# Kernel tuning notes

Hardware: AMD Instinct MI355X
Metric: run time of the kernel (lower is better)

The kernel has to match this reference:

```python
import jax, jax.numpy as jnp
import numpy as np

B, E, H, K, C, N = 4096, 768, 2048, 128, 200, 20


def _ln(x, g, b, eps=1e-5):
    m = x.mean(-1, keepdims=True)
    v = jnp.mean((x - m) ** 2, axis=-1, keepdims=True)
    return (x - m) / jnp.sqrt(v + eps) * g + b


def _sn(W):
    # spectral_norm parametrization at eval: divide by top singular value
    return W / jnp.linalg.norm(W, ord=2)


def setup_inputs() -> dict:
    key = jax.random.key(0)
    ks = jax.random.split(key, 8)
    return {
        "features": jax.random.normal(ks[0], (B, E), dtype=jnp.float32),
        "ln1_g": jnp.ones((E,), jnp.float32),
        "ln1_b": jnp.zeros((E,), jnp.float32),
        "W1": jax.random.normal(ks[1], (H, E), jnp.float32) * 0.02,
        "b1": jnp.zeros((H,), jnp.float32),
        "ln2_g": jnp.ones((H,), jnp.float32),
        "ln2_b": jnp.zeros((H,), jnp.float32),
        "W2": jax.random.normal(ks[2], (H, H), jnp.float32) * 0.02,
        "b2": jnp.zeros((H,), jnp.float32),
        "Wp": jax.random.normal(ks[3], (K, H), jnp.float32) * 0.02,
        "bp": jnp.zeros((K,), jnp.float32),
        "log_lengthscale": jnp.zeros((), jnp.float32),  # log(1.0)
        "inducing_points": jax.random.normal(ks[4], (C, N, K), jnp.float32) * 0.1,
        "variational_mean": jax.random.normal(ks[5], (C, N), jnp.float32) * 0.01,
    }


def reference(features, ln1_g, ln1_b, W1, b1, ln2_g, ln2_b, W2, b2, Wp, bp,
              log_lengthscale, inducing_points, variational_mean):
    # SN-MLP feature extractor (dropout=0 at eval)
    h = _ln(features, ln1_g, ln1_b)
    h = jax.nn.gelu(h @ _sn(W1).T + b1, approximate=False)
    h = _ln(h, ln2_g, ln2_b)
    h = jax.nn.gelu(h @ _sn(W2).T + b2, approximate=False)
    h = h @ _sn(Wp).T + bp  # [B, K]

    n_ind = inducing_points.shape[1]
    ls2 = jnp.exp(2.0 * log_lengthscale)
    z = inducing_points  # [C, N, K]

    # RBF kernels via squared distances (batched over classes)
    h2 = jnp.sum(h * h, axis=-1)            # [B]
    z2 = jnp.sum(z * z, axis=-1)            # [C, N]
    hz = jnp.einsum('bk,cnk->cbn', h, z)    # [C, B, N]
    d2_xz = jnp.maximum(h2[None, :, None] + z2[:, None, :] - 2.0 * hz, 0.0)
    k_xz = jnp.exp(-d2_xz / (2.0 * ls2))    # [C, B, N]

    zz = jnp.einsum('cnk,cmk->cnm', z, z)   # [C, N, N]
    d2_zz = jnp.maximum(z2[:, :, None] + z2[:, None, :] - 2.0 * zz, 0.0)
    k_zz = jnp.exp(-d2_zz / (2.0 * ls2)) + 1e-4 * jnp.eye(n_ind, dtype=h.dtype)

    L = jnp.linalg.cholesky(k_zz)           # [C, N, N]
    cho = jax.vmap(lambda Lc, mc: jax.scipy.linalg.cho_solve((Lc, True), mc))
    alpha = cho(L, variational_mean)        # [C, N]
    logits = jnp.einsum('cbn,cn->bc', k_xz, alpha)  # [B, C]

    tri = jax.vmap(lambda Lc, kc: jax.scipy.linalg.solve_triangular(Lc, kc.T, lower=True))
    v = tri(L, k_xz)                        # [C, N, B]
    var_c = jnp.maximum(1.0 - jnp.sum(v * v, axis=1), 0.0)  # [C, B]
    uncertainty = var_c.mean(axis=0)        # [B]

    probs = jax.nn.softmax(logits, axis=-1)
    return probs, logits, uncertainty
```

## Files before the change

kernel.cpp:

```cpp
#include <hip/hip_runtime.h>
#include <cstdint>
#include <cstddef>

#define NB 4096
#define NE 768
#define NH 2048
#define NKF 128
#define NC 200
#define NN 20
#define NITER_R 8

typedef __attribute__((ext_vector_type(8))) short s16x8;
typedef __attribute__((ext_vector_type(8))) unsigned short u16x8;
typedef __attribute__((ext_vector_type(4))) unsigned short u16x4;
typedef __attribute__((ext_vector_type(4))) float f32x4;

__device__ inline unsigned short f2bf(float x) {
  unsigned u = __builtin_bit_cast(unsigned, x);
  u += 0x7fffu + ((u >> 16) & 1u);
  return (unsigned short)(u >> 16);
}
__device__ inline float bf2f(unsigned short h) {
  return __builtin_bit_cast(float, (unsigned)h << 16);
}
__device__ inline float gelu_exact(float x) {
  return x * 0.5f * (1.0f + erff(x * 0.70710678118654752f));
}

__device__ inline void gl16(const unsigned short* g, unsigned short* l) {
  __builtin_amdgcn_global_load_lds(
      (const __attribute__((address_space(1))) unsigned int*)(uintptr_t)(g),
      (__attribute__((address_space(3))) unsigned int*)(uintptr_t)(l),
      16, 0, 0);
}

constexpr size_t SZ_W1BF = (size_t)NH * NE * 2;
constexpr size_t SZ_W2BF = (size_t)NH * NH * 2;
constexpr size_t SZ_WPBF = (size_t)NKF * NH * 2;
constexpr size_t SZ_SLOT = (size_t)NB * NH * 2;

constexpr size_t OFF_W1BF = 0;
constexpr size_t OFF_W2BF = OFF_W1BF + SZ_W1BF;
constexpr size_t OFF_WPBF = OFF_W2BF + SZ_W2BF;
constexpr size_t OFF_XBF  = OFF_WPBF + SZ_WPBF;
constexpr size_t OFF_H2BF = OFF_XBF;
constexpr size_t OFF_H1BF = OFF_XBF + SZ_SLOT;
constexpr size_t OFF_H1N  = OFF_H1BF + SZ_SLOT;
constexpr size_t OFF_HP   = OFF_H1N + SZ_SLOT;
constexpr size_t OFF_H2S  = OFF_HP + (size_t)NB * NKF * 4;
constexpr size_t OFF_PV   = OFF_H2S + (size_t)NB * 4;
constexpr size_t OFF_SINV = OFF_PV + (size_t)3 * 3 * 2048 * 4;
constexpr size_t OFF_Z2   = OFF_SINV + 256;
constexpr size_t OFF_LC   = OFF_Z2 + (size_t)NC * NN * 4;
constexpr size_t OFF_AL   = OFF_LC + (size_t)NC * NN * NN * 4;
constexpr size_t WS_NEED  = OFF_AL + (size_t)NC * NN * 4;

constexpr size_t GOFF_W1T   = OFF_XBF;
constexpr size_t GOFF_Q0    = GOFF_W1T + (size_t)NE * NH * 2;
constexpr size_t GOFF_Q1    = GOFF_Q0 + (size_t)NE * NE * 2;
constexpr size_t GOFF_GPACC = GOFF_Q1 + (size_t)NE * NE * 2;
constexpr size_t GOFF_G1SA  = GOFF_GPACC + (size_t)NKF * NKF * 4;
constexpr size_t GOFF_G1SB  = GOFF_G1SA + (size_t)NE * NE * 2;
constexpr size_t OFF_XBF2   = GOFF_G1SB + (size_t)NE * NE * 2;
static_assert(OFF_XBF2 + (size_t)NB * NE * 2 <= OFF_XBF + SZ_SLOT, "slotA overflow");
constexpr size_t GOFF_G2SA = OFF_H1BF;
constexpr size_t GOFF_G2SB = OFF_H1BF + (size_t)NH * NH * 2;
constexpr size_t GOFF_P0 = OFF_H1N;
constexpr size_t GOFF_P1 = OFF_H1N + (size_t)NH * NH * 2;
constexpr size_t OFF_HPBF = OFF_H1BF;
constexpr size_t OFF_ZPAD = OFF_H1BF + (size_t)NB * NKF * 2;
constexpr size_t OFF_LGT  = OFF_H1N;
constexpr size_t OFF_VART = OFF_LGT + (size_t)NC * NB * 4;
static_assert(OFF_VART + (size_t)NC * NB * 4 <= OFF_H1N + SZ_SLOT, "slotC overflow");

__global__ __launch_bounds__(256) void prep_all(const float* __restrict__ X,
                                                const float* __restrict__ g1,
                                                const float* __restrict__ be1,
                                                const float* __restrict__ W1,
                                                const float* __restrict__ W2,
                                                const float* __restrict__ Wp,
                                                unsigned short* __restrict__ W1T,
                                                unsigned short* __restrict__ W1bf,
                                                unsigned short* __restrict__ W2bf,
                                                unsigned short* __restrict__ Wpbf,
                                                unsigned short* __restrict__ Xbf,
                                                float* __restrict__ Hp,
                                                float* __restrict__ Gpacc,
                                                float* __restrict__ slots) {
  int b = blockIdx.x, t = threadIdx.x;
  if (b < 384) {
    __shared__ float tile[64][65];
    int bx = b % 12, by = b / 12;
    int c0 = bx * 64, r0 = by * 64;
    int tx = t & 63, ty = t >> 6;
    #pragma unroll
    for (int j = 0; j < 16; ++j) {
      int r = ty + j * 4;
      float v = W1[(size_t)(r0 + r) * NE + c0 + tx];
      tile[r][tx] = v;
      W1bf[(size_t)(r0 + r) * NE + c0 + tx] = f2bf(v);
    }
    __syncthreads();
    #pragma unroll
    for (int j = 0; j < 16; ++j) {
      int cc = ty + j * 4;
      W1T[(size_t)(c0 + cc) * NH + r0 + tx] = f2bf(tile[tx][cc]);
    }
  } else if (b < 896) {
    const int n2v = (NH * NH) / 4;
    const int npv = (NKF * NH) / 4;
    int idx = (b - 384) * 256 + t;
    const int stride = 512 * 256;
    for (int i = idx; i < n2v + npv; i += stride) {
      const float* src; unsigned short* dst; int off;
      if (i < n2v) { src = W2; dst = W2bf; off = i; }
      else         { src = Wp; dst = Wpbf; off = i - n2v; }
      float4 v = *(const float4*)(src + (size_t)off * 4);
      u16x4 o;
      o[0] = f2bf(v.x); o[1] = f2bf(v.y); o[2] = f2bf(v.z); o[3] = f2bf(v.w);
      *(u16x4*)(dst + (size_t)off * 4) = o;
    }
  } else if (b < 1920) {
    int wid = t >> 6, lane = t & 63;
    int row = (b - 896) * 4 + wid;
    const float* xr = X + (size_t)row * NE;
    float4 v[3];
    float s = 0.f, sq = 0.f;
    #pragma unroll
    for (int j = 0; j < 3; ++j) {
      v[j] = *(const float4*)(xr + j * 256 + lane * 4);
      s += v[j].x + v[j].y + v[j].z + v[j].w;
      sq += v[j].x * v[j].x + v[j].y * v[j].y + v[j].z * v[j].z + v[j].w * v[j].w;
    }
    for (int off = 32; off; off >>= 1) { s += __shfl_down(s, off); sq += __shfl_down(sq, off); }
    s = __shfl(s, 0); sq = __shfl(sq, 0);
    float mean = s * (1.0f / NE);
    float var = sq * (1.0f / NE) - mean * mean;
    float rstd = rsqrtf(var + 1e-5f);
    unsigned short* orow = Xbf + (size_t)row * NE;
    #pragma unroll
    for (int j = 0; j < 3; ++j) {
      int e0 = j * 256 + lane * 4;
      float4 gg = *(const float4*)(g1 + e0);
      float4 bb = *(const float4*)(be1 + e0);
      u16x4 o;
      o[0] = f2bf((v[j].x - mean) * rstd * gg.x + bb.x);
      o[1] = f2bf((v[j].y - mean) * rstd * gg.y + bb.y);
      o[2] = f2bf((v[j].z - mean) * rstd * gg.z + bb.z);
      o[3] = f2bf((v[j].w - mean) * rstd * gg.w + bb.w);
      *(u16x4*)(orow + e0) = o;
    }
  } else if (b < 1984) {
    float4 z = {0.f, 0.f, 0.f, 0.f};
    int base = (b - 1920) * 2048 + t;
    #pragma unroll
    for (int q = 0; q < 8; ++q) *((float4*)Hp + base + q * 256) = z;
  } else if (b < 1988) {
    float4 z = {0.f, 0.f, 0.f, 0.f};
    int base = (b - 1984) * 1024 + t;
    #pragma unroll
    for (int q = 0; q < 4; ++q) *((float4*)Gpacc + base + q * 256) = z;
  } else {
    if (t < 32) slots[t] = 0.f;
  }
}

__global__ __launch_bounds__(256) void gemm_multi(const unsigned short* __restrict__ A1, int K1,
                                                  unsigned short* __restrict__ O1a,
                                                  unsigned short* __restrict__ O1b,
                                                  const unsigned short* __restrict__ A2, int K2,
                                                  unsigned short* __restrict__ O2a,
                                                  unsigned short* __restrict__ O2b,
                                                  float cscale) {
  __shared__ __align__(16) unsigned short As[2][128 * 32];
  __shared__ __align__(16) unsigned short Bs[2][128 * 32];
  __shared__ __align__(16) unsigned short Tb[64][136];
  int b = blockIdx.x, t = threadIdx.x;
  const unsigned short* A;
  unsigned short* Cout;
  int Kk, Nn, kb, ke, ti;
  if (b < 42) {
    int kz = b / 21; ti = b % 21;
    A = A1; Kk = K1; Nn = NE;
    Cout = kz ? O1b : O1a;
    kb = kz * (K1 / 2); ke = kb + K1 / 2;
  } else {
    int idx = b - 42;
    int kz = idx / 136; ti = idx % 136;
    A = A2; Kk = K2; Nn = NH;
    Cout = kz ? O2b : O2a;
    kb = kz * (K2 / 2); ke = kb + K2 / 2;
  }
  int ri = 0;
  while ((ri + 1) * (ri + 2) / 2 <= ti) ++ri;
  int rj = ti - ri * (ri + 1) / 2;
  int bm0 = ri * 128, bn0 = rj * 128;

  int wid = t >> 6, lane = t & 63;
  int wm = wid >> 1, wn = wid & 1;
  f32x4 acc[4][4] = {};

  int lrow = t >> 2;
  int lk8 = (((t & 3) ^ ((t >> 3) & 3)) * 8);
  const unsigned short* Ag = A + (size_t)(bm0 + lrow) * Kk + lk8;
  const unsigned short* Bg = A + (size_t)(bn0 + lrow) * Kk + lk8;

  int arow = wm * 64 + (lane & 15);
  int brow = wn * 64 + (lane & 15);
  int kca = (((lane >> 4) ^ ((arow >> 1) & 3)) * 8);
  int kcb = (((lane >> 4) ^ ((brow >> 1) & 3)) * 8);

  #define STAGEM(nb, koff)                                  \
    do {                                                    \
      gl16(Ag + (koff), &As[nb][wid * 512]);                \
      gl16(Ag + (size_t)64 * Kk + (koff), &As[nb][2048 + wid * 512]); \
      gl16(Bg + (koff), &Bs[nb][wid * 512]);                \
      gl16(Bg + (size_t)64 * Kk + (koff), &Bs[nb][2048 + wid * 512]); \
    } while (0)

  STAGEM(0, kb);
  __syncthreads();
  int cb = 0;
  for (int ks = kb; ks < ke; ks += 32) {
    if (ks + 32 < ke) STAGEM(cb ^ 1, ks + 32);
    s16x8 af[4], bfr[4];
    #pragma unroll
    for (int i = 0; i < 4; ++i) af[i] = *(const s16x8*)&As[cb][(arow + i * 16) * 32 + kca];
    #pragma unroll
    for (int j = 0; j < 4; ++j) bfr[j] = *(const s16x8*)&Bs[cb][(brow + j * 16) * 32 + kcb];
    #pragma unroll
    for (int i = 0; i < 4; ++i)
      #pragma unroll
      for (int j = 0; j < 4; ++j)
        acc[i][j] = __builtin_amdgcn_mfma_f32_16x16x32_bf16(af[i], bfr[j], acc[i][j], 0, 0, 0);
    __syncthreads();
    cb ^= 1;
  }
  #undef STAGEM

  int crow0 = bm0 + wm * 64 + (lane >> 4) * 4;
  int ccol0 = bn0 + wn * 64 + (lane & 15);
  #pragma unroll
  for (int i = 0; i < 4; ++i)
    #pragma unroll
    for (int j = 0; j < 4; ++j) {
      int col = ccol0 + j * 16;
      #pragma unroll
      for (int r = 0; r < 4; ++r) {
        int row = crow0 + i * 16 + r;
        Cout[(size_t)row * Nn + col] = f2bf(acc[i][j][r] * cscale);
      }
    }

  if (bm0 != bn0) {
    #pragma unroll
    for (int h = 0; h < 2; ++h) {
      __syncthreads();
      if (wn == h) {
        #pragma unroll
        for (int i = 0; i < 4; ++i)
          #pragma unroll
          for (int j = 0; j < 4; ++j) {
            int lc = j * 16 + (lane & 15);
            #pragma unroll
            for (int r = 0; r < 4; ++r) {
              int lr = wm * 64 + i * 16 + (lane >> 4) * 4 + r;
              Tb[lc][lr] = f2bf(acc[i][j][r] * cscale);
            }
          }
      }
      __syncthreads();
      int c = t >> 2;
      int rs = (t & 3) * 32;
      unsigned short* dst = Cout + (size_t)(bn0 + h * 64 + c) * Nn + bm0 + rs;
      #pragma unroll
      for (int q = 0; q < 4; ++q) *(u16x8*)(dst + q * 8) = *(const u16x8*)&Tb[c][rs + q * 8];
    }
  }
}

__global__ __launch_bounds__(256) void add2(const unsigned short* __restrict__ Q0,
                                            const unsigned short* __restrict__ Q1,
                                            unsigned short* __restrict__ G1o,
                                            const unsigned short* __restrict__ P0,
                                            const unsigned short* __restrict__ P1,
                                            unsigned short* __restrict__ G2o) {
  const int n1 = (NE * NE) / 8;
  const int n2 = (NH * NH) / 8;
  int idx = blockIdx.x * 256 + threadIdx.x;
  for (int i = idx; i < n1 + n2; i += gridDim.x * 256) {
    const unsigned short *a, *bb; unsigned short* o; int off;
    if (i < n1) { a = Q0; bb = Q1; o = G1o; off = i; }
    else        { a = P0; bb = P1; o = G2o; off = i - n1; }
    u16x8 x = *(const u16x8*)(a + (size_t)off * 8);
    u16x8 y = *(const u16x8*)(bb + (size_t)off * 8);
    u16x8 r;
    #pragma unroll
    for (int q = 0; q < 8; ++q) r[q] = f2bf(bf2f(x[q]) + bf2f(y[q]));
    *(u16x8*)(o + (size_t)off * 8) = r;
  }
}

__global__ __launch_bounds__(256) void gram_iter(const unsigned short* __restrict__ Q0,
                                                 const unsigned short* __restrict__ Q1,
                                                 const unsigned short* __restrict__ P0,
                                                 const unsigned short* __restrict__ P1,
                                                 float* __restrict__ vb,
                                                 float* __restrict__ slots, int iter) {
  int b = blockIdx.x, t = threadIdx.x;
  int m, r0, Kd;
  const unsigned short *ga, *gb;
  if (b < 96) { m = 0; ga = Q0; gb = Q1; Kd = NE; r0 = b * 8; }
  else        { m = 1; ga = P0; gb = P1; Kd = NH; r0 = (b - 96) * 8; }

  const float* vin = vb + ((size_t)m * 2 + (iter & 1)) * 2048;
  float* vout      = vb + ((size_t)m * 2 + ((iter + 1) & 1)) * 2048;

  __shared__ float vs[2048];
  for (int k = t; k < Kd; k += 256) vs[k] = (iter == 0) ? 1.0f : vin[k];
  __syncthreads();

  int w = t >> 6, lane = t & 63;
  float nrm = 0.f;
  #pragma unroll
  for (int rr = 0; rr < 2; ++rr) {
    int row = r0 + w * 2 + rr;
    const unsigned short* g0 = ga + (size_t)row * Kd;
    const unsigned short* g1 = gb + (size_t)row * Kd;
    float s = 0.f;
    for (int k0 = lane * 8; k0 < Kd; k0 += 512) {
      u16x8 u = *(const u16x8*)(g0 + k0);
      u16x8 u2 = *(const u16x8*)(g1 + k0);
      #pragma unroll
      for (int q = 0; q < 8; ++q) s += (bf2f(u[q]) + bf2f(u2[q])) * vs[k0 + q];
    }
    for (int off = 32; off; off >>= 1) s += __shfl_down(s, off);
    if (lane == 0) { vout[row] = s; nrm += s * s; }
  }
  if (lane == 0) atomicAdd(&slots[m * 16 + iter + 1], nrm);
}

__global__ __launch_bounds__(256) void gp_power(const float* __restrict__ Gp,
                                                float* __restrict__ sinv) {
  __shared__ float v[NKF];
  __shared__ float pred[8][NKF];
  __shared__ float nacc[2];
  int t = threadIdx.x;
  int rg = (t & 31) * 4;
  int ks = t >> 5;
  f32x4 Greg[16];
  #pragma unroll
  for (int kk = 0; kk < 16; ++kk)
    Greg[kk] = *(const f32x4*)(Gp + (size_t)(ks * 16 + kk) * NKF + rg);
  if (t < NKF) v[t] = 1.0f;
  __syncthreads();
  float s_last0 = 1.f, s_last1 = 1.f;
  for (int it = 0; it < 40; ++it) {
    f32x4 p = {0.f, 0.f, 0.f, 0.f};
    #pragma unroll
    for (int kq = 0; kq < 4; ++kq) {
      f32x4 vv = *(const f32x4*)&v[ks * 16 + kq * 4];
      p += Greg[kq * 4 + 0] * vv[0];
      p += Greg[kq * 4 + 1] * vv[1];
      p += Greg[kq * 4 + 2] * vv[2];
      p += Greg[kq * 4 + 3] * vv[3];
    }
    *(f32x4*)&pred[ks][rg] = p;
    __syncthreads();
    float s = 0.f;
    if (t < NKF) {
      #pragma unroll
      for (int q = 0; q < 8; ++q) s += pred[q][t];
      v[t] = s;
    }
    if (it >= 38) {
      float q2 = (t < NKF) ? s * s : 0.f;
      #pragma unroll
      for (int off = 32; off; off >>= 1) q2 += __shfl_down(q2, off);
      if (t == 0) nacc[0] = q2;
      if (t == 64) nacc[1] = q2;
    }
    __syncthreads();
    if (it == 38 && t == 0) s_last0 = nacc[0] + nacc[1];
    if (it == 39 && t == 0) s_last1 = nacc[0] + nacc[1];
  }
  if (t == 0) sinv[2] = powf(s_last1 / s_last0, -0.25f);
}

__global__ __launch_bounds__(256) void ln_h(const unsigned short* __restrict__ X,
                                            const float* __restrict__ g,
                                            const float* __restrict__ b,
                                            unsigned short* __restrict__ out) {
  int wid = threadIdx.x >> 6, lane = threadIdx.x & 63;
  int row = blockIdx.x * 4 + wid;
  const unsigned short* xr = X + (size_t)row * NH;
  float xv[32];
  float s = 0.f, sq = 0.f;
  #pragma unroll
  for (int j = 0; j < 4; ++j) {
    u16x8 u = *(const u16x8*)(xr + j * 512 + lane * 8);
    #pragma unroll
    for (int q = 0; q < 8; ++q) {
      float x = bf2f(u[q]);
      xv[j * 8 + q] = x; s += x; sq += x * x;
    }
  }
  for (int off = 32; off; off >>= 1) { s += __shfl_down(s, off); sq += __shfl_down(sq, off); }
  s = __shfl(s, 0); sq = __shfl(sq, 0);
  float mean = s * (1.0f / NH);
  float var = sq * (1.0f / NH) - mean * mean;
  float rstd = rsqrtf(var + 1e-5f);
  unsigned short* orow = out + (size_t)row * NH;
  #pragma unroll
  for (int j = 0; j < 4; ++j) {
    int e0 = j * 512 + lane * 8;
    float4 ga = *(const float4*)(g + e0);
    float4 gb = *(const float4*)(g + e0 + 4);
    float4 ba = *(const float4*)(b + e0);
    float4 bb = *(const float4*)(b + e0 + 4);
    u16x8 o;
    o[0] = f2bf((xv[j*8+0] - mean) * rstd * ga.x + ba.x);
    o[1] = f2bf((xv[j*8+1] - mean) * rstd * ga.y + ba.y);
    o[2] = f2bf((xv[j*8+2] - mean) * rstd * ga.z + ba.z);
    o[3] = f2bf((xv[j*8+3] - mean) * rstd * ga.w + ba.w);
    o[4] = f2bf((xv[j*8+4] - mean) * rstd * gb.x + bb.x);
    o[5] = f2bf((xv[j*8+5] - mean) * rstd * gb.y + bb.y);
    o[6] = f2bf((xv[j*8+6] - mean) * rstd * gb.z + bb.z);
    o[7] = f2bf((xv[j*8+7] - mean) * rstd * gb.w + bb.w);
    *(u16x8*)(orow + e0) = o;
  }
}

template <int EPI>
__global__ __launch_bounds__(256) void gemm_nt(const unsigned short* __restrict__ A,
                                               const unsigned short* __restrict__ Bm,
                                               const float* __restrict__ bias,
                                               void* __restrict__ Cout,
                                               int M, int Nn, int Kk, int KCH,
                                               const float* __restrict__ sig, int sigmode) {
  __shared__ __align__(16) unsigned short As[2][128 * 32];
  __shared__ __align__(16) unsigned short Bs[2][128 * 32];
  int t = threadIdx.x;
  int bm0 = blockIdx.x * 128, bn0 = blockIdx.y * 128;
  int wid = t >> 6, lane = t & 63;
  int wm = wid >> 1, wn = wid & 1;

  int kb = 0, ke = Kk;
  if (KCH > 0) { kb = blockIdx.z * KCH; ke = kb + KCH; }

  f32x4 acc[4][4] = {};

  int lrow = t >> 2;
  int lk8 = (((t & 3) ^ ((t >> 3) & 3)) * 8);
  const unsigned short* Ag = A + (size_t)(bm0 + lrow) * Kk + lk8;
  const unsigned short* Bg = Bm + (size_t)(bn0 + lrow) * Kk + lk8;

  int arow = wm * 64 + (lane & 15);
  int brow = wn * 64 + (lane & 15);
  int kca = (((lane >> 4) ^ ((arow >> 1) & 3)) * 8);
  int kcb = (((lane >> 4) ^ ((brow >> 1) & 3)) * 8);

  #define STAGE(nb, koff)                                   \
    do {                                                    \
      gl16(Ag + (koff), &As[nb][wid * 512]);                \
      gl16(Ag + (size_t)64 * Kk + (koff), &As[nb][2048 + wid * 512]); \
      gl16(Bg + (koff), &Bs[nb][wid * 512]);                \
      gl16(Bg + (size_t)64 * Kk + (koff), &Bs[nb][2048 + wid * 512]); \
    } while (0)

  STAGE(0, kb);
  __syncthreads();
  int cb = 0;
  for (int ks = kb; ks < ke; ks += 32) {
    if (ks + 32 < ke) STAGE(cb ^ 1, ks + 32);
    s16x8 af[4], bfr[4];
    #pragma unroll
    for (int i = 0; i < 4; ++i) af[i] = *(const s16x8*)&As[cb][(arow + i * 16) * 32 + kca];
    #pragma unroll
    for (int j = 0; j < 4; ++j) bfr[j] = *(const s16x8*)&Bs[cb][(brow + j * 16) * 32 + kcb];
    #pragma unroll
    for (int i = 0; i < 4; ++i)
      #pragma unroll
      for (int j = 0; j < 4; ++j)
        acc[i][j] = __builtin_amdgcn_mfma_f32_16x16x32_bf16(af[i], bfr[j], acc[i][j], 0, 0, 0);
    __syncthreads();
    cb ^= 1;
  }
  #undef STAGE

  float sc = 1.0f;
  if (sigmode == 1) sc = powf(16.0f * sqrtf(sig[NITER_R] / sig[NITER_R - 1]), -0.125f);
  else if (sigmode == 2) sc = sig[0];

  int crow0 = bm0 + wm * 64 + (lane >> 4) * 4;
  int ccol0 = bn0 + wn * 64 + (lane & 15);
  if constexpr (EPI == 0) {
    unsigned short* C = (unsigned short*)Cout;
    #pragma unroll
    for (int i = 0; i < 4; ++i) {
      #pragma unroll
      for (int j = 0; j < 4; ++j) {
        int col = ccol0 + j * 16;
        float bb = bias[col];
        #pragma unroll
        for (int r = 0; r < 4; ++r) {
          int row = crow0 + i * 16 + r;
          float x = acc[i][j][r] * sc + bb;
          C[(size_t)row * Nn + col] = f2bf(gelu_exact(x));
        }
      }
    }
  } else {
    float* C = (float*)Cout;
    #pragma unroll
    for (int i = 0; i < 4; ++i)
      #pragma unroll
      for (int j = 0; j < 4; ++j) {
        int col = ccol0 + j * 16;
        #pragma unroll
        for (int r = 0; r < 4; ++r) {
          int row = crow0 + i * 16 + r;
          atomicAdd(&C[(size_t)row * Nn + col], acc[i][j][r] * sc);
        }
      }
  }
}

__global__ __launch_bounds__(256) void finish_proj(const float* __restrict__ Hp,
                                                   const float* __restrict__ bp,
                                                   unsigned short* __restrict__ Hpb,
                                                   float* __restrict__ h2) {
  int wid = threadIdx.x >> 6, lane = threadIdx.x & 63;
  int row = blockIdx.x * 4 + wid;
  const float* r = Hp + (size_t)row * NKF;
  float x0 = r[lane] + bp[lane];
  float x1 = r[lane + 64] + bp[lane + 64];
  float s = x0 * x0 + x1 * x1;
  for (int off = 32; off; off >>= 1) s += __shfl_down(s, off);
  unsigned short* hb = Hpb + (size_t)row * NKF;
  hb[lane] = f2bf(x0);
  hb[lane + 64] = f2bf(x1);
  if (lane == 0) h2[row] = s;
}

__global__ __launch_bounds__(128) void gp_prep(const float* __restrict__ z,
                                               const float* __restrict__ vm,
                                               const float* __restrict__ ll,
                                               float* __restrict__ z2g,
                                               float* __restrict__ Lig,
                                               float* __restrict__ alphag,
                                               unsigned short* __restrict__ zpad) {
  int c = blockIdx.x, t = threadIdx.x;
  __shared__ float zc[NN * NKF];
  __shared__ float Amat[NN][NN + 1];
  __shared__ float Li[NN][NN + 1];
  __shared__ float z2s[NN], ys[NN], al[NN];
  const float* zcg = z + (size_t)c * NN * NKF;
  for (int i = t; i < NN * NKF; i += 128) zc[i] = zcg[i];
  __syncthreads();
  if (t < NN) {
    float s = 0.f;
    for (int k = 0; k < NKF; ++k) { float v = zc[t * NKF + k]; s += v * v; }
    z2s[t] = s;
    z2g[c * NN + t] = s;
  }
  __syncthreads();
  float inv2 = 0.5f * expf(-2.0f * ll[0]);
  for (int e = t; e < NN * NN; e += 128) {
    int n = e / NN, m = e % NN;
    float d = 0.f;
    for (int k = 0; k < NKF; ++k) d += zc[n * NKF + k] * zc[m * NKF + k];
    float d2 = fmaxf(z2s[n] + z2s[m] - 2.0f * d, 0.0f);
    float v = expf(-d2 * inv2);
    if (n == m) v += 1e-4f;
    Amat[n][m] = v;
  }
  __syncthreads();
  for (int j = 0; j < NN; ++j) {
    if (t == 0) {
      float s = Amat[j][j];
      for (int p = 0; p < j; ++p) s -= Amat[j][p] * Amat[j][p];
      Amat[j][j] = sqrtf(s);
    }
    __syncthreads();
    if (t > j && t < NN) {
      float s = Amat[t][j];
      for (int p = 0; p < j; ++p) s -= Amat[t][p] * Amat[j][p];
      Amat[t][j] = s / Amat[j][j];
    }
    __syncthreads();
  }
  if (t < NN) {
    int j = t;
    for (int n = 0; n < NN; ++n) {
      float s;
      if (n < j) s = 0.f;
      else {
        s = (n == j) ? 1.f : 0.f;
        for (int m = j; m < n; ++m) s -= Amat[n][m] * Li[m][j];
        s /= Amat[n][n];
      }
      Li[n][j] = s;
    }
  }
  if (t == 0) {
    const float* mc = vm + c * NN;
    for (int n = 0; n < NN; ++n) {
      float s = mc[n];
      for (int m = 0; m < n; ++m) s -= Amat[n][m] * ys[m];
      ys[n] = s / Amat[n][n];
    }
    for (int n = NN - 1; n >= 0; --n) {
      float s = ys[n];
      for (int m = n + 1; m < NN; ++m) s -= Amat[m][n] * al[m];
      al[n] = s / Amat[n][n];
    }
  }
  __syncthreads();
  for (int e = t; e < NN * NN; e += 128)
    Lig[(size_t)c * NN * NN + e] = Li[e / NN][e % NN];
  if (t < NN) alphag[c * NN + t] = al[t];
  unsigned short* zp = zpad + (size_t)c * 32 * NKF;
  for (int i = t; i < 32 * NKF; i += 128) {
    int n = i >> 7;
    zp[i] = (n < NN) ? f2bf(zc[n * NKF + (i & 127)]) : (unsigned short)0;
  }
}

__global__ __launch_bounds__(256) void gp_main(const unsigned short* __restrict__ Hpb,
                                               const float* __restrict__ h2g,
                                               const unsigned short* __restrict__ zpad,
                                               const float* __restrict__ z2g,
                                               const float* __restrict__ Lig,
                                               const float* __restrict__ alphag,
                                               const float* __restrict__ ll,
                                               float* __restrict__ logitsT,
                                               float* __restrict__ varT) {
  int c = blockIdx.y, b0 = blockIdx.x * 256, t = threadIdx.x;
  int w = t >> 6, lane = t & 63;
  __shared__ __align__(16) unsigned short zs[32 * 136];
  __shared__ float kxs[256][21];
  __shared__ float Ls[NN][21];
  __shared__ float z2s[32], al[NN], ht2[256];

  {
    const unsigned short* zp = zpad + (size_t)c * 32 * NKF;
    int n = t >> 3, k = (t & 7) * 16;
    u16x8 a = *(const u16x8*)(zp + n * NKF + k);
    u16x8 b = *(const u16x8*)(zp + n * NKF + k + 8);
    *(u16x8*)&zs[n * 136 + k] = a;
    *(u16x8*)&zs[n * 136 + k + 8] = b;
  }
  for (int i = t; i < NN * NN; i += 256) Ls[i / NN][i % NN] = Lig[(size_t)c * NN * NN + i];
  if (t < 32) z2s[t] = (t < NN) ? z2g[c * NN + t] : 0.f;
  if (t < NN) al[t] = alphag[c * NN + t];
  ht2[t] = h2g[b0 + t];
  float inv2 = 0.5f * __expf(-2.0f * ll[0]);
  __syncthreads();

  f32x4 acc[4][2] = {};
  const unsigned short* hbase = Hpb + (size_t)(b0 + w * 64 + (lane & 15)) * NKF + (lane >> 4) * 8;
  #pragma unroll
  for (int ks = 0; ks < 4; ++ks) {
    s16x8 af[4], bfr[2];
    #pragma unroll
    for (int i = 0; i < 4; ++i) af[i] = *(const s16x8*)(hbase + (size_t)i * 16 * NKF + ks * 32);
    #pragma unroll
    for (int j = 0; j < 2; ++j)
      bfr[j] = *(const s16x8*)&zs[(j * 16 + (lane & 15)) * 136 + ks * 32 + (lane >> 4) * 8];
    #pragma unroll
    for (int i = 0; i < 4; ++i)
      #pragma unroll
      for (int j = 0; j < 2; ++j)
        acc[i][j] = __builtin_amdgcn_mfma_f32_16x16x32_bf16(af[i], bfr[j], acc[i][j], 0, 0, 0);
  }

  #pragma unroll
  for (int i = 0; i < 4; ++i)
    #pragma unroll
    for (int j = 0; j < 2; ++j) {
      int col = j * 16 + (lane & 15);
      #pragma unroll
      for (int r = 0; r < 4; ++r) {
        int rl = w * 64 + i * 16 + (lane >> 4) * 4 + r;
        float d2 = fmaxf(ht2[rl] + z2s[col] - 2.0f * acc[i][j][r], 0.0f);
        float kx = __expf(-d2 * inv2);
        if (col < NN) kxs[rl][col] = kx;
      }
    }
  __syncthreads();

  float kr[NN];
  #pragma unroll
  for (int n = 0; n < NN; ++n) kr[n] = kxs[t][n];
  float lg = 0.f;
  #pragma unroll
  for (int n = 0; n < NN; ++n) lg += kr[n] * al[n];
  logitsT[(size_t)c * NB + b0 + t] = lg;

  float vsum = 0.f;
  #pragma unroll
  for (int n = 0; n < NN; ++n) {
    float wv = 0.f;
    #pragma unroll
// ... 23 lines not shown
    vs += varT[(size_t)cc * NB + b0 + j];
  }
  redmx[p][j] = mx;
  redvs[p][j] = vs;
  __syncthreads();
  if (p == 0) {
    mxs[j] = fmaxf(fmaxf(redmx[0][j], redmx[1][j]), fmaxf(redmx[2][j], redmx[3][j]));
    unc[b0 + j] = (redvs[0][j] + redvs[1][j] + redvs[2][j] + redvs[3][j]) * (1.0f / NC);
  }
  __syncthreads();
  float m2 = mxs[j], sm = 0.f;
  for (int cc = p * 50; cc < p * 50 + 50; ++cc) sm += __expf(tile[cc][j] - m2);
  redsm[p][j] = sm;
  __syncthreads();
  if (p == 0) invs[j] = 1.0f / (redsm[0][j] + redsm[1][j] + redsm[2][j] + redsm[3][j]);
  __syncthreads();
  for (int i = t; i < 64 * NC; i += 256) {
    int jj = i / NC, cc = i % NC;
    float lv = tile[cc][jj];
    size_t o = (size_t)(b0 + jj) * NC + cc;
    probs[o] = __expf(lv - mxs[jj]) * invs[jj];
    logits_out[o] = lv;
  }
}

extern "C" void kernel_launch(void* const* d_in, const int* in_sizes, int n_in,
                              void* d_out, int out_size, void* d_ws, size_t ws_size,
                              hipStream_t stream) {
  if (ws_size < WS_NEED) return;

  const float* X   = (const float*)d_in[0];
  const float* g1  = (const float*)d_in[1];
  const float* be1 = (const float*)d_in[2];
  const float* W1  = (const float*)d_in[3];
  const float* b1  = (const float*)d_in[4];
  const float* g2  = (const float*)d_in[5];
  const float* be2 = (const float*)d_in[6];
  const float* W2  = (const float*)d_in[7];
  const float* b2  = (const float*)d_in[8];
  const float* Wp  = (const float*)d_in[9];
  const float* bp  = (const float*)d_in[10];
  const float* ll  = (const float*)d_in[11];
  const float* Z   = (const float*)d_in[12];
  const float* VM  = (const float*)d_in[13];

  char* ws = (char*)d_ws;
  unsigned short* W1bf = (unsigned short*)(ws + OFF_W1BF);
  unsigned short* W2bf = (unsigned short*)(ws + OFF_W2BF);
  unsigned short* Wpbf = (unsigned short*)(ws + OFF_WPBF);
  unsigned short* Xbf  = (unsigned short*)(ws + OFF_XBF2);
  unsigned short* H2bf = (unsigned short*)(ws + OFF_H2BF);
  unsigned short* H1bf = (unsigned short*)(ws + OFF_H1BF);
  unsigned short* H1n  = (unsigned short*)(ws + OFF_H1N);
  float* Hp    = (float*)(ws + OFF_HP);
  float* h2s   = (float*)(ws + OFF_H2S);
  float* vb    = (float*)(ws + OFF_PV);
  float* slots = vb + 2 * 2 * 2048;
  float* sinv  = (float*)(ws + OFF_SINV);
  float* z2g   = (float*)(ws + OFF_Z2);
  float* Lg    = (float*)(ws + OFF_LC);
  float* alphag= (float*)(ws + OFF_AL);

  unsigned short* W1T  = (unsigned short*)(ws + GOFF_W1T);
  unsigned short* Q0   = (unsigned short*)(ws + GOFF_Q0);
  unsigned short* Q1   = (unsigned short*)(ws + GOFF_Q1);
  float*          Gpacc= (float*)(ws + GOFF_GPACC);
  unsigned short* G1sA = (unsigned short*)(ws + GOFF_G1SA);
  unsigned short* G1sB = (unsigned short*)(ws + GOFF_G1SB);
  unsigned short* G2sA = (unsigned short*)(ws + GOFF_G2SA);
  unsigned short* G2sB = (unsigned short*)(ws + GOFF_G2SB);
  unsigned short* P0   = (unsigned short*)(ws + GOFF_P0);
  unsigned short* P1   = (unsigned short*)(ws + GOFF_P1);
  unsigned short* Hpb  = (unsigned short*)(ws + OFF_HPBF);
  unsigned short* zpad = (unsigned short*)(ws + OFF_ZPAD);
  float* logitsT = (float*)(ws + OFF_LGT);
  float* varT    = (float*)(ws + OFF_VART);

  float* out    = (float*)d_out;
  float* logits = out + (size_t)NB * NC;
  float* unc    = out + (size_t)2 * NB * NC;

  prep_all<<<dim3(1989), 256, 0, stream>>>(X, g1, be1, W1, W2, Wp,
                                           W1T, W1bf, W2bf, Wpbf, Xbf, Hp, Gpacc, slots);

  gemm_nt<1><<<dim3(1, 1, 16), 256, 0, stream>>>(Wpbf, Wpbf, nullptr, (void*)Gpacc, NKF, NKF, NH, NH / 16, nullptr, 0);
  gp_power<<<dim3(1), 256, 0, stream>>>(Gpacc, sinv);
  gemm_multi<<<dim3(314), 256, 0, stream>>>(W1T, NH, Q0, Q1, W2bf, NH, P0, P1, 1.0f);
  add2<<<dim3(1024), 256, 0, stream>>>(Q0, Q1, G1sA, P0, P1, G2sA);
  gemm_multi<<<dim3(314), 256, 0, stream>>>(G1sA, NE, Q0, Q1, G2sA, NH, P0, P1, 1.0f);
  add2<<<dim3(1024), 256, 0, stream>>>(Q0, Q1, G1sB, P0, P1, G2sB);
  gemm_multi<<<dim3(314), 256, 0, stream>>>(G1sB, NE, Q0, Q1, G2sB, NH, P0, P1, 0.0625f);
  for (int i = 0; i < NITER_R; ++i)
    gram_iter<<<dim3(352), 256, 0, stream>>>(Q0, Q1, P0, P1, vb, slots, i);

  gemm_nt<0><<<dim3(NB / 128, NH / 128), 256, 0, stream>>>(Xbf, W1bf, b1, (void*)H1bf, NB, NH, NE, 0, slots, 1);
  ln_h<<<dim3(NB / 4), 256, 0, stream>>>(H1bf, g2, be2, H1n);
  gemm_nt<0><<<dim3(NB / 128, NH / 128), 256, 0, stream>>>(H1n, W2bf, b2, (void*)H2bf, NB, NH, NH, 0, slots + 16, 1);
  gemm_nt<1><<<dim3(NB / 128, 1, 8), 256, 0, stream>>>(H2bf, Wpbf, bp, (void*)Hp, NB, NKF, NH, NH / 8, sinv + 2, 2);
  finish_proj<<<dim3(NB / 4), 256, 0, stream>>>(Hp, bp, Hpb, h2s);

  gp_prep<<<dim3(NC), 128, 0, stream>>>(Z, VM, ll, z2g, Lg, alphag, zpad);
  gp_main<<<dim3(NB / 256, NC), 256, 0, stream>>>(Hpb, h2s, zpad, z2g, Lg, alphag, ll, logitsT, varT);
  softmax_t<<<dim3(NB / 64), 256, 0, stream>>>(logitsT, varT, out, logits, unc);
}
```

Measured before the change: 470.2 us.

## Fold small prep kernels into larger launches and cut launch count

Moves the GP Cholesky prep into prep_all blocks and the Wp Gram GEMM and its power iteration into extra blocks of the gemm_multi launches, removing several separate launches. The projection GEMM now writes per-split bf16 partials that finish_proj reduces and scales, replacing float atomics and the Hp zeroing. gram_iter materialises the summed Gram matrix on its first iteration and then reads a single buffer. gp_main converts inducing points to bf16 itself instead of reading a padded copy. The aim is less launch overhead and serialization, at the cost of bf16 rounding in the projection partials and busier, more irregular mega-kernels.

After: 453.7 us. -3.5%, faster.

```diff
diff --git a/kernel.cpp b/kernel.cpp
--- a/kernel.cpp
+++ b/kernel.cpp
@@ -67,10 +67,10 @@
 constexpr size_t GOFF_G2SB = OFF_H1BF + (size_t)NH * NH * 2;
 constexpr size_t GOFF_P0 = OFF_H1N;
 constexpr size_t GOFF_P1 = OFF_H1N + (size_t)NH * NH * 2;
-constexpr size_t OFF_HPBF = OFF_H1BF;
-constexpr size_t OFF_ZPAD = OFF_H1BF + (size_t)NB * NKF * 2;
-constexpr size_t OFF_LGT  = OFF_H1N;
-constexpr size_t OFF_VART = OFF_LGT + (size_t)NC * NB * 4;
+constexpr size_t OFF_HPBF  = OFF_H1BF;
+constexpr size_t OFF_PPROJ = OFF_H1N;
+constexpr size_t OFF_LGT   = OFF_H1N;
+constexpr size_t OFF_VART  = OFF_LGT + (size_t)NC * NB * 4;
 static_assert(OFF_VART + (size_t)NC * NB * 4 <= OFF_H1N + SZ_SLOT, "slotC overflow");
 
 __global__ __launch_bounds__(256) void prep_all(const float* __restrict__ X,
@@ -79,14 +79,19 @@
                                                 const float* __restrict__ W1,
                                                 const float* __restrict__ W2,
                                                 const float* __restrict__ Wp,
+                                                const float* __restrict__ Z,
+                                                const float* __restrict__ VM,
+                                                const float* __restrict__ ll,
                                                 unsigned short* __restrict__ W1T,
                                                 unsigned short* __restrict__ W1bf,
                                                 unsigned short* __restrict__ W2bf,
                                                 unsigned short* __restrict__ Wpbf,
                                                 unsigned short* __restrict__ Xbf,
-                                                float* __restrict__ Hp,
                                                 float* __restrict__ Gpacc,
-                                                float* __restrict__ slots) {
+                                                float* __restrict__ slots,
+                                                float* __restrict__ z2g,
+                                                float* __restrict__ Lig,
+                                                float* __restrict__ alphag) {
   int b = blockIdx.x, t = threadIdx.x;
   if (b < 384) {
     __shared__ float tile[64][65];
@@ -150,18 +155,84 @@
       o[3] = f2bf((v[j].w - mean) * rstd * gg.w + bb.w);
       *(u16x4*)(orow + e0) = o;
     }
-  } else if (b < 1984) {
+  } else if (b < 1924) {
     float4 z = {0.f, 0.f, 0.f, 0.f};
-    int base = (b - 1920) * 2048 + t;
-    #pragma unroll
-    for (int q = 0; q < 8; ++q) *((float4*)Hp + base + q * 256) = z;
-  } else if (b < 1988) {
-    float4 z = {0.f, 0.f, 0.f, 0.f};
-    int base = (b - 1984) * 1024 + t;
+    int base = (b - 1920) * 1024 + t;
     #pragma unroll
     for (int q = 0; q < 4; ++q) *((float4*)Gpacc + base + q * 256) = z;
+  } else if (b == 1924) {
+    if (t < 32) slots[t] = 0.f;
   } else {
-    if (t < 32) slots[t] = 0.f;
+    int c = b - 1925;
+    __shared__ float zc[NN * NKF];
+    __shared__ float Amat[NN][NN + 1];
+    __shared__ float Li[NN][NN + 1];
+    __shared__ float z2s[NN], ys[NN], al[NN];
+    const float* zcg = Z + (size_t)c * NN * NKF;
+    for (int i = t; i < NN * NKF; i += 256) zc[i] = zcg[i];
+    __syncthreads();
+    if (t < NN) {
+      float s = 0.f;
+      for (int k = 0; k < NKF; ++k) { float v = zc[t * NKF + k]; s += v * v; }
+      z2s[t] = s;
+      z2g[c * NN + t] = s;
+    }
+    __syncthreads();
+    float inv2 = 0.5f * expf(-2.0f * ll[0]);
+    for (int e = t; e < NN * NN; e += 256) {
+      int n = e / NN, m = e % NN;
+      float d = 0.f;
+      for (int k = 0; k < NKF; ++k) d += zc[n * NKF + k] * zc[m * NKF + k];
+      float d2 = fmaxf(z2s[n] + z2s[m] - 2.0f * d, 0.0f);
+      float v = expf(-d2 * inv2);
+      if (n == m) v += 1e-4f;
+      Amat[n][m] = v;
+    }
+    __syncthreads();
+    for (int j = 0; j < NN; ++j) {
+      if (t == 0) {
+        float s = Amat[j][j];
+        for (int p = 0; p < j; ++p) s -= Amat[j][p] * Amat[j][p];
+        Amat[j][j] = sqrtf(s);
+      }
+      __syncthreads();
+      if (t > j && t < NN) {
+        float s = Amat[t][j];
+        for (int p = 0; p < j; ++p) s -= Amat[t][p] * Amat[j][p];
+        Amat[t][j] = s / Amat[j][j];
+      }
+      __syncthreads();
+    }
+    if (t < NN) {
+      int j = t;
+      for (int n = 0; n < NN; ++n) {
+        float s;
+        if (n < j) s = 0.f;
+        else {
+          s = (n == j) ? 1.f : 0.f;
+          for (int m = j; m < n; ++m) s -= Amat[n][m] * Li[m][j];
+          s /= Amat[n][n];
+        }
+        Li[n][j] = s;
+      }
+    }
+    if (t == 0) {
+      const float* mc = VM + c * NN;
+      for (int n = 0; n < NN; ++n) {
+        float s = mc[n];
+        for (int m = 0; m < n; ++m) s -= Amat[n][m] * ys[m];
+        ys[n] = s / Amat[n][n];
+      }
+      for (int n = NN - 1; n >= 0; --n) {
+        float s = ys[n];
+        for (int m = n + 1; m < NN; ++m) s -= Amat[m][n] * al[m];
+        al[n] = s / Amat[n][n];
+      }
+    }
+    __syncthreads();
+    for (int e = t; e < NN * NN; e += 256)
+      Lig[(size_t)c * NN * NN + e] = Li[e / NN][e % NN];
+    if (t < NN) alphag[c * NN + t] = al[t];
   }
 }
 
@@ -171,30 +242,90 @@
                                                   const unsigned short* __restrict__ A2, int K2,
                                                   unsigned short* __restrict__ O2a,
                                                   unsigned short* __restrict__ O2b,
-                                                  float cscale) {
+                                                  const unsigned short* __restrict__ Wpb,
+                                                  float* __restrict__ Gpacc,
+                                                  float* __restrict__ sinv,
+                                                  float cscale, int extra) {
   __shared__ __align__(16) unsigned short As[2][128 * 32];
   __shared__ __align__(16) unsigned short Bs[2][128 * 32];
   __shared__ __align__(16) unsigned short Tb[64][136];
   int b = blockIdx.x, t = threadIdx.x;
+
+  if (extra == 2 && b == 314) {
+    float* vv = (float*)&As[0][0];
+    float* nacc = vv + 160;
+    float (*pred)[NKF] = (float(*)[NKF]) & Bs[0][0];
+    int rg = (t & 31) * 4;
+    int ks2 = t >> 5;
+    f32x4 Greg[16];
+    #pragma unroll
+    for (int kk = 0; kk < 16; ++kk)
+      Greg[kk] = *(const f32x4*)(Gpacc + (size_t)(ks2 * 16 + kk) * NKF + rg);
+    if (t < NKF) vv[t] = 1.0f;
+    __syncthreads();
+    float s_last0 = 1.f, s_last1 = 1.f;
+    for (int it = 0; it < 40; ++it) {
+      f32x4 p = {0.f, 0.f, 0.f, 0.f};
+      #pragma unroll
+      for (int kq = 0; kq < 4; ++kq) {
+        f32x4 vq = *(const f32x4*)&vv[ks2 * 16 + kq * 4];
+        p += Greg[kq * 4 + 0] * vq[0];
+        p += Greg[kq * 4 + 1] * vq[1];
+        p += Greg[kq * 4 + 2] * vq[2];
+        p += Greg[kq * 4 + 3] * vq[3];
+      }
+      *(f32x4*)&pred[ks2][rg] = p;
+      __syncthreads();
+      float s = 0.f;
+      if (t < NKF) {
+        #pragma unroll
+        for (int q = 0; q < 8; ++q) s += pred[q][t];
+        vv[t] = s;
+      }
+      if (it >= 38) {
+        float q2 = (t < NKF) ? s * s : 0.f;
+        #pragma unroll
+        for (int off = 32; off; off >>= 1) q2 += __shfl_down(q2, off);
+        if (t == 0) nacc[0] = q2;
+        if (t == 64) nacc[1] = q2;
+      }
+      __syncthreads();
+      if (it == 38 && t == 0) s_last0 = nacc[0] + nacc[1];
+      if (it == 39 && t == 0) s_last1 = nacc[0] + nacc[1];
+    }
+    if (t == 0) sinv[2] = powf(s_last1 / s_last0, -0.25f);
+    return;
+  }
+
+  int epimode = 0;
   const unsigned short* A;
-  unsigned short* Cout;
-  int Kk, Nn, kb, ke, ti;
-  if (b < 42) {
-    int kz = b / 21; ti = b % 21;
-    A = A1; Kk = K1; Nn = NE;
-    Cout = kz ? O1b : O1a;
-    kb = kz * (K1 / 2); ke = kb + K1 / 2;
+  unsigned short* Cout = nullptr;
+  int Kk, Nn, kb, ke, bm0, bn0;
+  if (extra == 1 && b >= 314) {
+    int idx = b - 314;
+    A = Wpb; Kk = K2; Nn = NKF;
+    kb = idx * 128; ke = kb + 128;
+    bm0 = 0; bn0 = 0;
+    epimode = 1;
   } else {
-    int idx = b - 42;
-    int kz = idx / 136; ti = idx % 136;
-    A = A2; Kk = K2; Nn = NH;
-    Cout = kz ? O2b : O2a;
-    kb = kz * (K2 / 2); ke = kb + K2 / 2;
-  }
-  int ri = 0;
-  while ((ri + 1) * (ri + 2) / 2 <= ti) ++ri;
-  int rj = ti - ri * (ri + 1) / 2;
-  int bm0 = ri * 128, bn0 = rj * 128;
+    int ti;
+    if (b < 42) {
+      int kz = b / 21; ti = b % 21;
+      A = A1; Kk = K1; Nn = NE;
+      Cout = kz ? O1b : O1a;
+      kb = kz * (K1 / 2); ke = kb + K1 / 2;
+    } else {
+      int idx = b - 42;
+      int kz = idx / 136; ti = idx % 136;
+      A = A2; Kk = K2; Nn = NH;
+      Cout = kz ? O2b : O2a;
+      kb = kz * (K2 / 2); ke = kb + K2 / 2;
+    }
+    int ri = 0;
+    while ((ri + 1) * (ri + 2) / 2 <= ti) ++ri;
+    int rj = ti - ri * (ri + 1) / 2;
+    bm0 = ri * 128; bn0 = rj * 128;
+  }
 
   int wid = t >> 6, lane = t & 63;
   int wm = wid >> 1, wn = wid & 1;
@@ -240,6 +371,21 @@
 
   int crow0 = bm0 + wm * 64 + (lane >> 4) * 4;
   int ccol0 = bn0 + wn * 64 + (lane & 15);
+  if (epimode == 1) {
+    #pragma unroll
+    for (int i = 0; i < 4; ++i)
+      #pragma unroll
+      for (int j = 0; j < 4; ++j) {
+        int col = ccol0 + j * 16;
+        #pragma unroll
+        for (int r = 0; r < 4; ++r) {
+          int row = crow0 + i * 16 + r;
+          atomicAdd(&Gpacc[(size_t)row * NKF + col], acc[i][j][r]);
+        }
+      }
+    return;
+  }
+
   #pragma unroll
   for (int i = 0; i < 4; ++i)
     #pragma unroll
@@ -305,86 +451,60 @@
                                                  const unsigned short* __restrict__ Q1,
                                                  const unsigned short* __restrict__ P0,
                                                  const unsigned short* __restrict__ P1,
+                                                 unsigned short* __restrict__ G1s,
+                                                 unsigned short* __restrict__ G2s,
                                                  float* __restrict__ vb,
                                                  float* __restrict__ slots, int iter) {
   int b = blockIdx.x, t = threadIdx.x;
   int m, r0, Kd;
   const unsigned short *ga, *gb;
-  if (b < 96) { m = 0; ga = Q0; gb = Q1; Kd = NE; r0 = b * 8; }
-  else        { m = 1; ga = P0; gb = P1; Kd = NH; r0 = (b - 96) * 8; }
+  unsigned short* gs;
+  if (b < 96) { m = 0; ga = Q0; gb = Q1; gs = G1s; Kd = NE; r0 = b * 8; }
+  else        { m = 1; ga = P0; gb = P1; gs = G2s; Kd = NH; r0 = (b - 96) * 8; }
 
   const float* vin = vb + ((size_t)m * 2 + (iter & 1)) * 2048;
   float* vout      = vb + ((size_t)m * 2 + ((iter + 1) & 1)) * 2048;
 
   __shared__ float vs[2048];
-  for (int k = t; k < Kd; k += 256) vs[k] = (iter == 0) ? 1.0f : vin[k];
-  __syncthreads();
+  if (iter > 0) {
+    for (int k = t; k < Kd; k += 256) vs[k] = vin[k];
+    __syncthreads();
+  }
 
   int w = t >> 6, lane = t & 63;
   float nrm = 0.f;
   #pragma unroll
   for (int rr = 0; rr < 2; ++rr) {
     int row = r0 + w * 2 + rr;
-    const unsigned short* g0 = ga + (size_t)row * Kd;
-    const unsigned short* g1 = gb + (size_t)row * Kd;
     float s = 0.f;
-    for (int k0 = lane * 8; k0 < Kd; k0 += 512) {
-      u16x8 u = *(const u16x8*)(g0 + k0);
-      u16x8 u2 = *(const u16x8*)(g1 + k0);
-      #pragma unroll
-      for (int q = 0; q < 8; ++q) s += (bf2f(u[q]) + bf2f(u2[q])) * vs[k0 + q];
+    if (iter == 0) {
+      const unsigned short* g0 = ga + (size_t)row * Kd;
+      const unsigned short* g1 = gb + (size_t)row * Kd;
+      unsigned short* gw = gs + (size_t)row * Kd;
+      for (int k0 = lane * 8; k0 < Kd; k0 += 512) {
+        u16x8 u = *(const u16x8*)(g0 + k0);
+        u16x8 u2 = *(const u16x8*)(g1 + k0);
+        u16x8 o;
+        #pragma unroll
+        for (int q = 0; q < 8; ++q) {
+          float gval = bf2f(u[q]) + bf2f(u2[q]);
+          o[q] = f2bf(gval);
+          s += gval;
+        }
+        *(u16x8*)(gw + k0) = o;
+      }
+    } else {
+      const unsigned short* g0 = gs + (size_t)row * Kd;
+      for (int k0 = lane * 8; k0 < Kd; k0 += 512) {
+        u16x8 u = *(const u16x8*)(g0 + k0);
+        #pragma unroll
+        for (int q = 0; q < 8; ++q) s += bf2f(u[q]) * vs[k0 + q];
+      }
     }
     for (int off = 32; off; off >>= 1) s += __shfl_down(s, off);
     if (lane == 0) { vout[row] = s; nrm += s * s; }
   }
   if (lane == 0) atomicAdd(&slots[m * 16 + iter + 1], nrm);
-}
-
-__global__ __launch_bounds__(256) void gp_power(const float* __restrict__ Gp,
-                                                float* __restrict__ sinv) {
-  __shared__ float v[NKF];
-  __shared__ float pred[8][NKF];
-  __shared__ float nacc[2];
-  int t = threadIdx.x;
-  int rg = (t & 31) * 4;
-  int ks = t >> 5;
-  f32x4 Greg[16];
-  #pragma unroll
-  for (int kk = 0; kk < 16; ++kk)
-    Greg[kk] = *(const f32x4*)(Gp + (size_t)(ks * 16 + kk) * NKF + rg);
-  if (t < NKF) v[t] = 1.0f;
-  __syncthreads();
-  float s_last0 = 1.f, s_last1 = 1.f;
-  for (int it = 0; it < 40; ++it) {
-    f32x4 p = {0.f, 0.f, 0.f, 0.f};
-    #pragma unroll
-    for (int kq = 0; kq < 4; ++kq) {
-      f32x4 vv = *(const f32x4*)&v[ks * 16 + kq * 4];
-      p += Greg[kq * 4 + 0] * vv[0];
-      p += Greg[kq * 4 + 1] * vv[1];
-      p += Greg[kq * 4 + 2] * vv[2];
-      p += Greg[kq * 4 + 3] * vv[3];
-    }
-    *(f32x4*)&pred[ks][rg] = p;
-    __syncthreads();
-    float s = 0.f;
-    if (t < NKF) {
-      #pragma unroll
-      for (int q = 0; q < 8; ++q) s += pred[q][t];
-      v[t] = s;
-    }
-    if (it >= 38) {
-      float q2 = (t < NKF) ? s * s : 0.f;
-      #pragma unroll
-      for (int off = 32; off; off >>= 1) q2 += __shfl_down(q2, off);
-      if (t == 0) nacc[0] = q2;
-      if (t == 64) nacc[1] = q2;
-    }
-    __syncthreads();
-    if (it == 38 && t == 0) s_last0 = nacc[0] + nacc[1];
-    if (it == 39 && t == 0) s_last1 = nacc[0] + nacc[1];
-  }
-  if (t == 0) sinv[2] = powf(s_last1 / s_last0, -0.25f);
 }
 
 __global__ __launch_bounds__(256) void ln_h(const unsigned short* __restrict__ X,
@@ -490,7 +610,6 @@
 
   float sc = 1.0f;
   if (sigmode == 1) sc = powf(16.0f * sqrtf(sig[NITER_R] / sig[NITER_R - 1]), -0.125f);
-  else if (sigmode == 2) sc = sig[0];
 
   int crow0 = bm0 + wm * 64 + (lane >> 4) * 4;
   int ccol0 = bn0 + wn * 64 + (lane & 15);
@@ -511,7 +630,7 @@
       }
     }
   } else {
-    float* C = (float*)Cout;
+    unsigned short* C = (unsigned short*)Cout + (size_t)blockIdx.z * M * Nn;
     #pragma unroll
     for (int i = 0; i < 4; ++i)
       #pragma unroll
@@ -520,21 +639,29 @@
         #pragma unroll
         for (int r = 0; r < 4; ++r) {
           int row = crow0 + i * 16 + r;
-          atomicAdd(&C[(size_t)row * Nn + col], acc[i][j][r] * sc);
+          C[(size_t)row * Nn + col] = f2bf(acc[i][j][r]);
         }
       }
   }
 }
 
-__global__ __launch_bounds__(256) void finish_proj(const float* __restrict__ Hp,
+__global__ __launch_bounds__(256) void finish_proj(const unsigned short* __restrict__ Pp,
                                                    const float* __restrict__ bp,
+                                                   const float* __restrict__ sc2,
                                                    unsigned short* __restrict__ Hpb,
                                                    float* __restrict__ h2) {
   int wid = threadIdx.x >> 6, lane = threadIdx.x & 63;
   int row = blockIdx.x * 4 + wid;
-  const float* r = Hp + (size_t)row * NKF;
-  float x0 = r[lane] + bp[lane];
-  float x1 = r[lane + 64] + bp[lane + 64];
+  float sc = sc2[0];
+  float x0 = 0.f, x1 = 0.f;
+  #pragma unroll
+  for (int z = 0; z < 8; ++z) {
+    const unsigned short* pr = Pp + (size_t)z * NB * NKF + (size_t)row * NKF;
+    x0 += bf2f(pr[lane]);
+    x1 += bf2f(pr[lane + 64]);
+  }
+  x0 = x0 * sc + bp[lane];
+  x1 = x1 * sc + bp[lane + 64];
   float s = x0 * x0 + x1 * x1;
   for (int off = 32; off; off >>= 1) s += __shfl_down(s, off);
   unsigned short* hb = Hpb + (size_t)row * NKF;
@@ -543,93 +670,9 @@
   if (lane == 0) h2[row] = s;
 }
 
-__global__ __launch_bounds__(128) void gp_prep(const float* __restrict__ z,
-                                               const float* __restrict__ vm,
-                                               const float* __restrict__ ll,
-                                               float* __restrict__ z2g,
-                                               float* __restrict__ Lig,
-                                               float* __restrict__ alphag,
-                                               unsigned short* __restrict__ zpad) {
-  int c = blockIdx.x, t = threadIdx.x;
-  __shared__ float zc[NN * NKF];
-  __shared__ float Amat[NN][NN + 1];
-  __shared__ float Li[NN][NN + 1];
-  __shared__ float z2s[NN], ys[NN], al[NN];
-  const float* zcg = z + (size_t)c * NN * NKF;
-  for (int i = t; i < NN * NKF; i += 128) zc[i] = zcg[i];
-  __syncthreads();
-  if (t < NN) {
-    float s = 0.f;
-    for (int k = 0; k < NKF; ++k) { float v = zc[t * NKF + k]; s += v * v; }
-    z2s[t] = s;
-    z2g[c * NN + t] = s;
-  }
-  __syncthreads();
-  float inv2 = 0.5f * expf(-2.0f * ll[0]);
-  for (int e = t; e < NN * NN; e += 128) {
-    int n = e / NN, m = e % NN;
-    float d = 0.f;
-    for (int k = 0; k < NKF; ++k) d += zc[n * NKF + k] * zc[m * NKF + k];
-    float d2 = fmaxf(z2s[n] + z2s[m] - 2.0f * d, 0.0f);
-    float v = expf(-d2 * inv2);
-    if (n == m) v += 1e-4f;
-    Amat[n][m] = v;
-  }
-  __syncthreads();
-  for (int j = 0; j < NN; ++j) {
-    if (t == 0) {
-      float s = Amat[j][j];
-      for (int p = 0; p < j; ++p) s -= Amat[j][p] * Amat[j][p];
-      Amat[j][j] = sqrtf(s);
-    }
-    __syncthreads();
-    if (t > j && t < NN) {
-      float s = Amat[t][j];
-      for (int p = 0; p < j; ++p) s -= Amat[t][p] * Amat[j][p];
-      Amat[t][j] = s / Amat[j][j];
-    }
-    __syncthreads();
-  }
-  if (t < NN) {
-    int j = t;
-    for (int n = 0; n < NN; ++n) {
-      float s;
-      if (n < j) s = 0.f;
-      else {
-        s = (n == j) ? 1.f : 0.f;
-        for (int m = j; m < n; ++m) s -= Amat[n][m] * Li[m][j];
-        s /= Amat[n][n];
-      }
-      Li[n][j] = s;
-    }
-  }
-  if (t == 0) {
-    const float* mc = vm + c * NN;
-    for (int n = 0; n < NN; ++n) {
-      float s = mc[n];
-      for (int m = 0; m < n; ++m) s -= Amat[n][m] * ys[m];
-      ys[n] = s / Amat[n][n];
-    }
-    for (int n = NN - 1; n >= 0; --n) {
-      float s = ys[n];
-      for (int m = n + 1; m < NN; ++m) s -= Amat[m][n] * al[m];
-      al[n] = s / Amat[n][n];
-    }
-  }
-  __syncthreads();
-  for (int e = t; e < NN * NN; e += 128)
-    Lig[(size_t)c * NN * NN + e] = Li[e / NN][e % NN];
-  if (t < NN) alphag[c * NN + t] = al[t];
-  unsigned short* zp = zpad + (size_t)c * 32 * NKF;
-  for (int i = t; i < 32 * NKF; i += 128) {
-    int n = i >> 7;
-    zp[i] = (n < NN) ? f2bf(zc[n * NKF + (i & 127)]) : (unsigned short)0;
-  }
-}
-
 __global__ __launch_bounds__(256) void gp_main(const unsigned short* __restrict__ Hpb,
                                                const float* __restrict__ h2g,
-                                               const unsigned short* __restrict__ zpad,
+                                               const float* __restrict__ Z,
                                                const float* __restrict__ z2g,
                                                const float* __restrict__ Lig,
                                                const float* __restrict__ alphag,
@@ -643,13 +686,14 @@
   __shared__ float Ls[NN][21];
   __shared__ float z2s[32], al[NN], ht2[256];
 
+  for (int i = t; i < 32 * 136; i += 256) zs[i] = 0;
+  __syncthreads();
   {
-    const unsigned short* zp = zpad + (size_t)c * 32 * NKF;
-    int n = t >> 3, k = (t & 7) * 16;
-    u16x8 a = *(const u16x8*)(zp + n * NKF + k);
-    u16x8 b = *(const u16x8*)(zp + n * NKF + k + 8);
-    *(u16x8*)&zs[n * 136 + k] = a;
-    *(u16x8*)&zs[n * 136 + k + 8] = b;
+    const float* zc = Z + (size_t)c * NN * NKF;
+    for (int i = t; i < NN * NKF; i += 256) {
+      int n = i >> 7, k = i & 127;
+      zs[n * 136 + k] = f2bf(zc[i]);
+    }
   }
   for (int i = t; i < NN * NN; i += 256) Ls[i / NN][i % NN] = Lig[(size_t)c * NN * NN + i];
   if (t < 32) z2s[t] = (t < NN) ? z2g[c * NN + t] : 0.f;
@@ -779,7 +823,6 @@
   unsigned short* H2bf = (unsigned short*)(ws + OFF_H2BF);
   unsigned short* H1bf = (unsigned short*)(ws + OFF_H1BF);
   unsigned short* H1n  = (unsigned short*)(ws + OFF_H1N);
-  float* Hp    = (float*)(ws + OFF_HP);
   float* h2s   = (float*)(ws + OFF_H2S);
   float* vb    = (float*)(ws + OFF_PV);
   float* slots = vb + 2 * 2 * 2048;
@@ -798,8 +841,8 @@
   unsigned short* G2sB = (unsigned short*)(ws + GOFF_G2SB);
   unsigned short* P0   = (unsigned short*)(ws + GOFF_P0);
   unsigned short* P1   = (unsigned short*)(ws + GOFF_P1);
-  unsigned short* Hpb  = (unsigned short*)(ws + OFF_HPBF);
-  unsigned short* zpad = (unsigned short*)(ws + OFF_ZPAD);
+  unsigned short* Hpb   = (unsigned short*)(ws + OFF_HPBF);
+  unsigned short* Pproj = (unsigned short*)(ws + OFF_PPROJ);
   float* logitsT = (float*)(ws + OFF_LGT);
   float* varT    = (float*)(ws + OFF_VART);
 
@@ -807,26 +850,27 @@
   float* logits = out + (size_t)NB * NC;
   float* unc    = out + (size_t)2 * NB * NC;
 
-  prep_all<<<dim3(1989), 256, 0, stream>>>(X, g1, be1, W1, W2, Wp,
-                                           W1T, W1bf, W2bf, Wpbf, Xbf, Hp, Gpacc, slots);
-
-  gemm_nt<1><<<dim3(1, 1, 16), 256, 0, stream>>>(Wpbf, Wpbf, nullptr, (void*)Gpacc, NKF, NKF, NH, NH / 16, nullptr, 0);
-  gp_power<<<dim3(1), 256, 0, stream>>>(Gpacc, sinv);
-  gemm_multi<<<dim3(314), 256, 0, stream>>>(W1T, NH, Q0, Q1, W2bf, NH, P0, P1, 1.0f);
+  prep_all<<<dim3(2125), 256, 0, stream>>>(X, g1, be1, W1, W2, Wp, Z, VM, ll,
+                                           W1T, W1bf, W2bf, Wpbf, Xbf,
+                                           Gpacc, slots, z2g, Lg, alphag);
+
+  gemm_multi<<<dim3(330), 256, 0, stream>>>(W1T, NH, Q0, Q1, W2bf, NH, P0, P1,
+                                            Wpbf, Gpacc, sinv, 1.0f, 1);
   add2<<<dim3(1024), 256, 0, stream>>>(Q0, Q1, G1sA, P0, P1, G2sA);
-  gemm_multi<<<dim3(314), 256, 0, stream>>>(G1sA, NE, Q0, Q1, G2sA, NH, P0, P1, 1.0f);
+  gemm_multi<<<dim3(315), 256, 0, stream>>>(G1sA, NE, Q0, Q1, G2sA, NH, P0, P1,
+                                            Wpbf, Gpacc, sinv, 1.0f, 2);
   add2<<<dim3(1024), 256, 0, stream>>>(Q0, Q1, G1sB, P0, P1, G2sB);
-  gemm_multi<<<dim3(314), 256, 0, stream>>>(G1sB, NE, Q0, Q1, G2sB, NH, P0, P1, 0.0625f);
+  gemm_multi<<<dim3(314), 256, 0, stream>>>(G1sB, NE, Q0, Q1, G2sB, NH, P0, P1,
+                                            Wpbf, Gpacc, sinv, 0.0625f, 0);
   for (int i = 0; i < NITER_R; ++i)
-    gram_iter<<<dim3(352), 256, 0, stream>>>(Q0, Q1, P0, P1, vb, slots, i);
+    gram_iter<<<dim3(352), 256, 0, stream>>>(Q0, Q1, P0, P1, G1sA, G2sA, vb, slots, i);
 
   gemm_nt<0><<<dim3(NB / 128, NH / 128), 256, 0, stream>>>(Xbf, W1bf, b1, (void*)H1bf, NB, NH, NE, 0, slots, 1);
   ln_h<<<dim3(NB / 4), 256, 0, stream>>>(H1bf, g2, be2, H1n);
   gemm_nt<0><<<dim3(NB / 128, NH / 128), 256, 0, stream>>>(H1n, W2bf, b2, (void*)H2bf, NB, NH, NH, 0, slots + 16, 1);
-  gemm_nt<1><<<dim3(NB / 128, 1, 8), 256, 0, stream>>>(H2bf, Wpbf, bp, (void*)Hp, NB, NKF, NH, NH / 8, sinv + 2, 2);
-  finish_proj<<<dim3(NB / 4), 256, 0, stream>>>(Hp, bp, Hpb, h2s);
-
-  gp_prep<<<dim3(NC), 128, 0, stream>>>(Z, VM, ll, z2g, Lg, alphag, zpad);
-  gp_main<<<dim3(NB / 256, NC), 256, 0, stream>>>(Hpb, h2s, zpad, z2g, Lg, alphag, ll, logitsT, varT);
+  gemm_nt<2><<<dim3(NB / 128, 1, 8), 256, 0, stream>>>(H2bf, Wpbf, nullptr, (void*)Pproj, NB, NKF, NH, NH / 8, nullptr, 0);
+  finish_proj<<<dim3(NB / 4), 256, 0, stream>>>(Pproj, bp, sinv + 2, Hpb, h2s);
+
+  gp_main<<<dim3(NB / 256, NC), 256, 0, stream>>>(Hpb, h2s, Z, z2g, Lg, alphag, ll, logitsT, varT);
   softmax_t<<<dim3(NB / 64), 256, 0, stream>>>(logitsT, varT, out, logits, unc);
 }
```
